# Kernel optimization log

Measured on AMD Instinct MI355X. Metric: run time of the kernel, lower is better.

Reference implementation:

```python
import jax, jax.numpy as jnp
import numpy as np

# ---- config (YOLOv4-style, TRAIN_SIZE=608, P2..P5) ----
STRIDES = (4.0, 8.0, 16.0, 32.0)
ANCHORS = np.array([
    [[12, 16], [19, 36], [40, 28], [36, 75]],
    [[36, 75], [76, 55], [72, 146], [142, 110]],
    [[72, 146], [142, 110], [192, 243], [459, 401]],
    [[142, 110], [192, 243], [300, 300], [459, 401]],
], dtype=np.float32)  # [LEVELS, NUM_ANCHORS, 2]
MAX_PROP = 100
SCORE_THRESH = 0.25
IOU_THRESH = 0.5


def decode_prediction(p, anchors, stride):
    # p: [b, A, h, w, 6] -> [b, A*h*w, 5] with xyxy + score
    b, A, h, w, _ = p.shape
    txy, twh, conf, cls = p[..., :2], p[..., 2:4], p[..., 4:5], p[..., 5:6]
    gx, gy = jnp.meshgrid(jnp.arange(w, dtype=p.dtype), jnp.arange(h, dtype=p.dtype))
    grid = jnp.stack([gx, gy], axis=-1)[None, None]  # [1,1,h,w,2]
    xy = (jax.nn.sigmoid(txy) + grid) * stride
    wh = jnp.exp(twh) * anchors[None, :, None, None, :]
    score = jax.nn.sigmoid(conf) * jax.nn.sigmoid(cls)
    x1y1 = xy - 0.5 * wh
    x2y2 = xy + 0.5 * wh
    out = jnp.concatenate([x1y1, x2y2, score], axis=-1)  # [b,A,h,w,5]
    return out.reshape(b, A * h * w, 5)


def _iou_one_vs_all(box, boxes):
    # box: [4], boxes: [N,4] (xyxy)
    lt = jnp.maximum(box[:2], boxes[:, :2])
    rb = jnp.minimum(box[2:], boxes[:, 2:])
    wh = jnp.maximum(rb - lt, 0.0)
    inter = wh[:, 0] * wh[:, 1]
    a1 = jnp.maximum(box[2] - box[0], 0.0) * jnp.maximum(box[3] - box[1], 0.0)
    a2 = jnp.maximum(boxes[:, 2] - boxes[:, 0], 0.0) * jnp.maximum(boxes[:, 3] - boxes[:, 1], 0.0)
    return inter / (a1 + a2 - inter + 1e-9)


def _nms_single(boxes, scores):
    # greedy NMS, padded to MAX_PROP with zero rows
    s0 = jnp.where(scores >= SCORE_THRESH, scores, 0.0)

    def step(s, _):
        i = jnp.argmax(s)
        sc = s[i]
        box = boxes[i]
        keep = sc > 0.0
        row = jnp.where(keep, jnp.concatenate([box, sc[None]]), jnp.zeros(5, boxes.dtype))
        iou = _iou_one_vs_all(box, boxes)
        s = jnp.where((iou > IOU_THRESH) & keep, 0.0, s)
        s = s.at[i].set(0.0)
        return s, row

    _, props = jax.lax.scan(step, s0, None, length=MAX_PROP)
    return props  # [MAX_PROP, 5]


def entry_stop_gradients(t, mask):
    # gradient flows only through entries where mask==1
    return jax.lax.stop_gradient(t) * (1.0 - mask) + t * mask


def _forward(p2, p3, p4, p5):
    anchors = jnp.asarray(ANCHORS)
    d2 = decode_prediction(p2, anchors[0], STRIDES[0])
    d3 = decode_prediction(p3, anchors[1], STRIDES[1])
    d4 = decode_prediction(p4, anchors[2], STRIDES[2])
    d5 = decode_prediction(p5, anchors[3], STRIDES[3])
    proposals = jnp.concatenate([d2, d3, d4, d5], axis=1)  # [b, N, 5]
    proposals = jax.vmap(lambda pr: _nms_single(pr[:, :4], pr[:, 4]))(proposals)  # [b, MAX_PROP, 5]
    mask = (jnp.sum(proposals[..., :4], axis=-1) != 0.0).astype(proposals.dtype)[..., None]
    return entry_stop_gradients(proposals, mask)


def setup_inputs() -> dict:
    key = jax.random.key(0)
    k2, k3, k4, k5 = jax.random.split(key, 4)
    b, A, ch = 32, 4, 6
    return {
        "p2": jax.random.normal(k2, (b, A, 152, 152, ch), dtype=jnp.float32),
        "p3": jax.random.normal(k3, (b, A, 76, 76, ch), dtype=jnp.float32),
        "p4": jax.random.normal(k4, (b, A, 38, 38, ch), dtype=jnp.float32),
        "p5": jax.random.normal(k5, (b, A, 19, 19, ch), dtype=jnp.float32),
    }


def reference(p2, p3, p4, p5):
    return _forward(p2, p3, p4, p5)
```

## Files before the change

kernel.cpp:

```cpp
#include <hip/hip_runtime.h>
#include <cstdint>
#include <cstddef>

typedef unsigned int u32;
typedef unsigned long long u64;

#define NTOT 122740
#define NQ   30685
#define NPAIR 61370
#define KTOP 1024
#define WIN  256
#define NBIN 4096
#define SCORE_T 0.25f
#define TBITS 0x3E800000u
#define CSTRIDE 64


#define WS_COUNTERS 524288
#define WS_COMPACT  532480
#define WS_SCORES   794624

__device__ __forceinline__ float sigm(float x) { return 1.0f / (1.0f + expf(-x)); }

__device__ __forceinline__ int score_bin(u32 bits) {
  return min(4095, 1 + (int)((bits - TBITS) >> 12));
}

__device__ __forceinline__ u64 shfl_u64(u64 x, int src) {
  int lo = __shfl((int)(u32)x, src, 64);
  int hi = __shfl((int)(u32)(x >> 32), src, 64);
  return ((u64)(u32)hi << 32) | (u32)lo;
}

__device__ float4 decode_box_from_gidx(u32 gidx, int b,
    const float* __restrict__ p2, const float* __restrict__ p3,
    const float* __restrict__ p4, const float* __restrict__ p5)
{
  const float* p; int t, H, W; float stride;
  float aw0, ah0, aw1, ah1, aw2, ah2, aw3, ah3;
  if (gidx < 92416u) {
    p = p2 + (size_t)b * 92416 * 6; t = (int)gidx; H = 152; W = 152; stride = 4.0f;
    aw0=12.f; ah0=16.f; aw1=19.f; ah1=36.f; aw2=40.f; ah2=28.f; aw3=36.f; ah3=75.f;
  } else if (gidx < 115520u) {
    p = p3 + (size_t)b * 23104 * 6; t = (int)(gidx - 92416u); H = 76; W = 76; stride = 8.0f;
    aw0=36.f; ah0=75.f; aw1=76.f; ah1=55.f; aw2=72.f; ah2=146.f; aw3=142.f; ah3=110.f;
  } else if (gidx < 121296u) {
    p = p4 + (size_t)b * 5776 * 6; t = (int)(gidx - 115520u); H = 38; W = 38; stride = 16.0f;
    aw0=72.f; ah0=146.f; aw1=142.f; ah1=110.f; aw2=192.f; ah2=243.f; aw3=459.f; ah3=401.f;
  } else {
    p = p5 + (size_t)b * 1444 * 6; t = (int)(gidx - 121296u); H = 19; W = 19; stride = 32.0f;
    aw0=142.f; ah0=110.f; aw1=192.f; ah1=243.f; aw2=300.f; ah2=300.f; aw3=459.f; ah3=401.f;
  }
  int HW = H * W;
  int a = t / HW;
  int r = t - a * HW;
  int y = r / W;
  int x = r - y * W;
  const float* q = p + (size_t)t * 6;
  float2 t01 = *(const float2*)(q + 0);
  float2 t23 = *(const float2*)(q + 2);
  float cx = (sigm(t01.x) + (float)x) * stride;
  float cy = (sigm(t01.y) + (float)y) * stride;
  float aw = (a == 0) ? aw0 : (a == 1) ? aw1 : (a == 2) ? aw2 : aw3;
  float ah = (a == 0) ? ah0 : (a == 1) ? ah1 : (a == 2) ? ah2 : ah3;
  float bw = expf(t23.x) * aw;
  float bh = expf(t23.y) * ah;
  return make_float4(cx - 0.5f * bw, cy - 0.5f * bh, cx + 0.5f * bw, cy + 0.5f * bh);
}

__device__ __forceinline__ bool iou_gt(float4 A, float4 B) {
  float ltx = fmaxf(A.x, B.x), lty = fmaxf(A.y, B.y);
  float rbx = fminf(A.z, B.z), rby = fminf(A.w, B.w);
  float w = fmaxf(rbx - ltx, 0.0f), h = fmaxf(rby - lty, 0.0f);
  float inter = w * h;
  float a1 = fmaxf(A.z - A.x, 0.0f) * fmaxf(A.w - A.y, 0.0f);
  float a2 = fmaxf(B.z - B.x, 0.0f) * fmaxf(B.w - B.y, 0.0f);
  float iou = inter / (a1 + a2 - inter + 1e-9f);
  return iou > 0.5f;
}

__global__ __launch_bounds__(1024)
void zero_kernel(u32* w) {
  int t = blockIdx.x * 1024 + threadIdx.x;
  if (t < 133120) w[t] = 0u;
}

__global__ __launch_bounds__(256)
void decode_score_hist(const float* __restrict__ p2, const float* __restrict__ p3,
                       const float* __restrict__ p4, const float* __restrict__ p5,
                       u32* __restrict__ scores, u32* __restrict__ hist)
{
  __shared__ u32 lhist[NBIN];
  const int tid = threadIdx.x;
  const int b = blockIdx.y;
  for (int i = tid; i < NBIN; i += 256) lhist[i] = 0u;
  __syncthreads();

  uint2* srow = (uint2*)(scores + (size_t)b * NTOT);
  const int pbase = blockIdx.x * 2048;
  #pragma unroll 2
  for (int k = 0; k < 8; ++k) {
    int P = pbase + k * 256 + tid;
    if (P < NPAIR) {
      int t0 = 2 * P;
      const float* p; int l0, LN;
      if (t0 < 92416)       { p = p2; l0 = t0;          LN = 92416; }
      else if (t0 < 115520) { p = p3; l0 = t0 - 92416;  LN = 23104; }
      else if (t0 < 121296) { p = p4; l0 = t0 - 115520; LN = 5776;  }
      else                  { p = p5; l0 = t0 - 121296; LN = 1444;  }
      const float* q = p + ((size_t)b * LN + (size_t)l0) * 6 + 4;
      float4 v1 = *(const float4*)(q);
      float4 v2 = *(const float4*)(q + 4);
      float s0 = sigm(v1.x) * sigm(v1.y);
      float s1 = sigm(v2.z) * sigm(v2.w);
      u32 b0 = (s0 >= SCORE_T) ? __float_as_uint(s0) : 0u;
      u32 b1 = (s1 >= SCORE_T) ? __float_as_uint(s1) : 0u;
      srow[P] = make_uint2(b0, b1);
      if (b0) atomicAdd(&lhist[score_bin(b0)], 1u);
      if (b1) atomicAdd(&lhist[score_bin(b1)], 1u);
    }
  }
  __syncthreads();
  u32* gh = hist + (size_t)b * NBIN;
  for (int i = tid; i < NBIN; i += 256) {
    u32 v = lhist[i];
    if (v) atomicAdd(&gh[i], v);
  }
}

__global__ __launch_bounds__(256)
void scan_kernel(u32* __restrict__ hist, u32* __restrict__ counters)
{
  __shared__ u32 shist[NBIN];
  __shared__ u32 scan[256];
  __shared__ int s_B, s_n;
  const int tid = threadIdx.x;
  const int b = blockIdx.x;
  u32* gh = hist + (size_t)b * NBIN;
  for (int i = tid; i < NBIN; i += 256) shist[i] = gh[i];
  __syncthreads();

  u32 loc[16];
  u32 g = 0;
  const int base = tid * 16;
  #pragma unroll
  for (int k = 0; k < 16; ++k) { loc[k] = shist[base + k]; g += loc[k]; }
  scan[tid] = g;
  __syncthreads();
  for (int off = 1; off < 256; off <<= 1) {
    u32 v = (tid + off < 256) ? scan[tid + off] : 0u;
    __syncthreads();
    scan[tid] += v;
    __syncthreads();
  }
  if (tid == 0 && scan[0] <= (u32)KTOP) { s_B = 1; s_n = (int)scan[0]; }
  {
    u32 nxt = (tid < 255) ? scan[tid + 1] : 0u;
    if (scan[tid] > (u32)KTOP && nxt <= (u32)KTOP) {
      u32 c = nxt; int Bv = base + 16; u32 nv = nxt;
      for (int k = 15; k >= 0; --k) {
        c += loc[k];
        if (c <= (u32)KTOP) { Bv = base + k; nv = c; } else break;
      }
      s_B = Bv; s_n = (int)nv;
    }
  }
  {
    u32 s = (tid < 255) ? scan[tid + 1] : 0u;
    for (int k = 15; k >= 0; --k) { gh[base + k] = s; s += loc[k]; }
  }
  __syncthreads();
  if (tid == 0) {
    counters[(size_t)b * CSTRIDE]     = (u32)s_n;
    counters[(size_t)b * CSTRIDE + 1] = (u32)max(s_B, 1);
  }
}

__global__ __launch_bounds__(256)
void filter_kernel(const u32* __restrict__ scores, u32* __restrict__ binpos,
                   const u32* __restrict__ counters, uint2* __restrict__ compact)
{
  const int tid = threadIdx.x;
  const int b = blockIdx.y;
  const int B = (int)counters[(size_t)b * CSTRIDE + 1];
  u32* bp = binpos + (size_t)b * NBIN;
  uint2* crow = compact + (size_t)b * KTOP;
  const uint4* sp = (const uint4*)(scores + (size_t)b * NTOT);
  const int i0 = blockIdx.x * 2048;
  const int i1 = min(i0 + 2048, NQ);
  for (int i = i0 + tid; i < i1; i += 256) {
    uint4 v = sp[i];
    u32 c4[4] = { v.x, v.y, v.z, v.w };
    #pragma unroll
    for (int c = 0; c < 4; ++c) {
      u32 bits = c4[c];
      if (bits) {
        int bin = score_bin(bits);
        if (bin >= B) {
          u32 slot = atomicAdd(&bp[bin], 1u);
          if (slot < (u32)KTOP)
            crow[slot] = make_uint2(bits, (u32)(4 * i + c));
        }
      }
    }
  }
}

__global__ __launch_bounds__(1024, 1)
void sort_nms_kernel(const uint2* __restrict__ compact, const u32* __restrict__ counters,
                     const float* __restrict__ p2, const float* __restrict__ p3,
                     const float* __restrict__ p4, const float* __restrict__ p5,
                     float* __restrict__ out)
{
  const int b = blockIdx.x;
  const int tid = threadIdx.x;

  __shared__ u64 skey[KTOP];
  __shared__ float4 sbox[WIN];
  __shared__ u64 smat[WIN * 4];
  __shared__ float4 selbox[100];
  __shared__ int s_misc[4];
  __shared__ int s_flag;

  const int n = min((int)counters[(size_t)b * CSTRIDE], KTOP);
  const uint2* crow = compact + (size_t)b * KTOP;

  if (tid < n) {
    uint2 pr = crow[tid];
    skey[tid] = ((u64)pr.x << 32) | (u32)(~pr.y);
  } else {
    skey[tid] = 0ull;
  }
  __syncthreads();

  for (int round = 0; round < 600; ++round) {
    if (tid == 0) s_flag = 0;
    __syncthreads();
    if (tid < 512) {
      int p = 2 * tid;
      u64 a = skey[p], c = skey[p + 1];
      if (a < c) { skey[p] = c; skey[p + 1] = a; s_flag = 1; }
    }
    __syncthreads();
    if (tid < 511) {
      int p = 2 * tid + 1;
      u64 a = skey[p], c = skey[p + 1];
      if (a < c) { skey[p] = c; skey[p + 1] = a; s_flag = 1; }
    }
    __syncthreads();
    int f = s_flag;
    __syncthreads();
    if (!f) break;
  }

  const int Wn = min(n, WIN);

  if (tid < WIN) {
    sbox[tid] = (tid < Wn) ? decode_box_from_gidx(~(u32)skey[tid], b, p2, p3, p4, p5)
                           : make_float4(0.f, 0.f, 0.f, 0.f);
  }
  __syncthreads();

  {
    int row = tid & 255, word = tid >> 8;
    u64 bits = 0;
    if (row < Wn) {
      float4 A = sbox[row];
      int j0 = word * 64;
      int je = min(64, Wn - j0);
      for (int j = 0; j < je; ++j)
        if (iou_gt(A, sbox[j0 + j])) bits |= (1ull << j);
    }
    smat[word * 256 + row] = bits;
  }
  __syncthreads();

  if (tid < 64) {
    const int lane = tid;
    u64 m0[4], m1[4], m2[4], m3[4];
    #pragma unroll
    for (int w = 0; w < 4; ++w) {
      m0[w] = smat[w * 256 +   0 + lane];
      m1[w] = smat[w * 256 +  64 + lane];
      m2[w] = smat[w * 256 + 128 + lane];
      m3[w] = smat[w * 256 + 192 + lane];
    }
    u64 live[4];
    #pragma unroll
    for (int g2 = 0; g2 < 4; ++g2) {
      int lo = g2 * 64;
      live[g2] = (Wn >= lo + 64) ? ~0ull : (Wn > lo ? ((1ull << (Wn - lo)) - 1ull) : 0ull);
    }
    int sel = 0;
    #pragma unroll 1
    for (int w2 = 0; w2 < 4; ++w2) {
      while (live[w2] && sel < 100) {
        int j = (int)__ffsll(live[w2]) - 1;
        int p = (w2 << 6) + j;
        u64 r0, r1, r2, r3;
        if (w2 == 0)      { r0 = shfl_u64(m0[0], j); r1 = shfl_u64(m0[1], j); r2 = shfl_u64(m0[2], j); r3 = shfl_u64(m0[3], j); }
        else if (w2 == 1) { r0 = shfl_u64(m1[0], j); r1 = shfl_u64(m1[1], j); r2 = shfl_u64(m1[2], j); r3 = shfl_u64(m1[3], j); }
        else if (w2 == 2) { r0 = shfl_u64(m2[0], j); r1 = shfl_u64(m2[1], j); r2 = shfl_u64(m2[2], j); r3 = shfl_u64(m2[3], j); }
        else              { r0 = shfl_u64(m3[0], j); r1 = shfl_u64(m3[1], j); r2 = shfl_u64(m3[2], j); r3 = shfl_u64(m3[3], j); }
        live[0] &= ~r0; live[1] &= ~r1; live[2] &= ~r2; live[3] &= ~r3;
        live[w2] &= ~(1ull << j);
        if (lane == 0) {
          float4 box = sbox[p];
          u64 k = skey[p];
          float sc = __uint_as_float((u32)(k >> 32));
          selbox[sel] = box;
          float* orow = out + (size_t)b * 500 + (size_t)sel * 5;
          orow[0] = box.x; orow[1] = box.y; orow[2] = box.z; orow[3] = box.w; orow[4] = sc;
        }
        sel++;
      }
    }
    if (lane == 0) {
      s_misc[2] = sel;
      s_misc[3] = (sel < 100 && n > WIN) ? 1 : 0;
    }
  }
  __syncthreads();

  if (s_misc[3]) {
    if (tid < 64) {
      const int lane = tid;
      int sel = s_misc[2];
      for (int p = WIN; p < n && sel < 100; ++p) {
        u64 k = skey[p];
        float4 box = decode_box_from_gidx(~(u32)k, b, p2, p3, p4, p5);
        bool hit = false;
        if (lane < sel) hit = iou_gt(selbox[lane], box);
        if (lane + 64 < sel) hit = hit || iou_gt(selbox[lane + 64], box);
        u64 anyhit = __ballot(hit);
        if (anyhit == 0ull) {
          if (lane == 0) {
            selbox[sel] = box;
            float sc = __uint_as_float((u32)(k >> 32));
            float* orow = out + (size_t)b * 500 + (size_t)sel * 5;
            orow[0] = box.x; orow[1] = box.y; orow[2] = box.z; orow[3] = box.w; orow[4] = sc;
          }
          sel++;
        }
      }
      if (lane == 0) s_misc[2] = sel;
    }
  }
  __syncthreads();

  const int nsel = s_misc[2];
  for (int i = tid; i < (100 - nsel) * 5; i += 1024)
    out[(size_t)b * 500 + (size_t)nsel * 5 + i] = 0.0f;
}

extern "C" void kernel_launch(void* const* d_in, const int* in_sizes, int n_in,
                              void* d_out, int out_size, void* d_ws, size_t ws_size,
                              hipStream_t stream) {
  const float* p2 = (const float*)d_in[0];
  const float* p3 = (const float*)d_in[1];
  const float* p4 = (const float*)d_in[2];
  const float* p5 = (const float*)d_in[3];
  float* out = (float*)d_out;

  unsigned char* w = (unsigned char*)d_ws;
  u32*   hist     = (u32*)w;
  u32*   counters = (u32*)(w + WS_COUNTERS);
  uint2* compact  = (uint2*)(w + WS_COMPACT);
  u32*   scores   = (u32*)(w + WS_SCORES);

  zero_kernel<<<130, 1024, 0, stream>>>(hist);
  decode_score_hist<<<dim3(30, 32), 256, 0, stream>>>(p2, p3, p4, p5, scores, hist);
  scan_kernel<<<32, 256, 0, stream>>>(hist, counters);
  filter_kernel<<<dim3(15, 32), 256, 0, stream>>>(scores, hist, counters, compact);
  sort_nms_kernel<<<32, 1024, 0, stream>>>(compact, counters, p2, p3, p4, p5, out);
}
```

Baseline: 189.7 us.

## Fuse scan, filter and sort-NMS into one per-batch kernel with bin-rank sort

Merges the histogram scan, top-K filter and sort/NMS stages into a single 1024-thread block per batch, keeping bin cursors and candidate keys in shared memory. The odd-even transposition sort is replaced by a rank sort within each histogram bin, which relies on bins already being ordered. The zeroing kernel becomes a memset. This removes launch overhead, global compact/counter traffic and many barrier-heavy sort rounds, but the filter pass now runs on only 32 blocks, reducing parallelism for scanning the score array.

Measured after the change: 184.6 us. 1.03x faster.

```diff
diff --git a/kernel.cpp b/kernel.cpp
--- a/kernel.cpp
+++ b/kernel.cpp
@@ -13,12 +13,9 @@
 #define NBIN 4096
 #define SCORE_T 0.25f
 #define TBITS 0x3E800000u
-#define CSTRIDE 64
-
-
-#define WS_COUNTERS 524288
-#define WS_COMPACT  532480
-#define WS_SCORES   794624
+
+
+#define WS_SCORES 524288
 
 __device__ __forceinline__ float sigm(float x) { return 1.0f / (1.0f + expf(-x)); }
 
@@ -77,12 +74,6 @@
   float a2 = fmaxf(B.z - B.x, 0.0f) * fmaxf(B.w - B.y, 0.0f);
   float iou = inter / (a1 + a2 - inter + 1e-9f);
   return iou > 0.5f;
-}
-
-__global__ __launch_bounds__(1024)
-void zero_kernel(u32* w) {
-  int t = blockIdx.x * 1024 + threadIdx.x;
-  if (t < 133120) w[t] = 0u;
 }
 
 __global__ __launch_bounds__(256)
@@ -128,35 +119,50 @@
   }
 }
 
-__global__ __launch_bounds__(256)
-void scan_kernel(u32* __restrict__ hist, u32* __restrict__ counters)
+__global__ __launch_bounds__(1024, 1)
+void mega_kernel(const u32* __restrict__ scores, const u32* __restrict__ hist,
+                 const float* __restrict__ p2, const float* __restrict__ p3,
+                 const float* __restrict__ p4, const float* __restrict__ p5,
+                 float* __restrict__ out)
 {
-  __shared__ u32 shist[NBIN];
-  __shared__ u32 scan[256];
+  const int b = blockIdx.x;
+  const int tid = threadIdx.x;
+
+  __shared__ u32 sstart[NBIN];
+  __shared__ u32 scur[NBIN];
+  __shared__ u32 sscan[256];
+  __shared__ u64 skey[KTOP];
+  __shared__ u64 skey2[KTOP];
+  __shared__ float4 sbox[WIN];
+  __shared__ u64 smat[WIN * 4];
+  __shared__ float4 selbox[100];
+  __shared__ int s_misc[4];
   __shared__ int s_B, s_n;
-  const int tid = threadIdx.x;
-  const int b = blockIdx.x;
-  u32* gh = hist + (size_t)b * NBIN;
-  for (int i = tid; i < NBIN; i += 256) shist[i] = gh[i];
-  __syncthreads();
-
-  u32 loc[16];
-  u32 g = 0;
-  const int base = tid * 16;
-  #pragma unroll
-  for (int k = 0; k < 16; ++k) { loc[k] = shist[base + k]; g += loc[k]; }
-  scan[tid] = g;
+
+  const u32* gh = hist + (size_t)b * NBIN;
+  for (int i = tid; i < NBIN; i += 1024) scur[i] = gh[i];
+  __syncthreads();
+
+  u32 loc[16]; int base = 0;
+  if (tid < 256) {
+    base = tid * 16;
+    u32 g = 0;
+    #pragma unroll
+    for (int k = 0; k < 16; ++k) { loc[k] = scur[base + k]; g += loc[k]; }
+    sscan[tid] = g;
+  }
   __syncthreads();
   for (int off = 1; off < 256; off <<= 1) {
-    u32 v = (tid + off < 256) ? scan[tid + off] : 0u;
+    u32 v = 0;
+    if (tid < 256) v = (tid + off < 256) ? sscan[tid + off] : 0u;
     __syncthreads();
-    scan[tid] += v;
+    if (tid < 256) sscan[tid] += v;
     __syncthreads();
   }
-  if (tid == 0 && scan[0] <= (u32)KTOP) { s_B = 1; s_n = (int)scan[0]; }
-  {
-    u32 nxt = (tid < 255) ? scan[tid + 1] : 0u;
-    if (scan[tid] > (u32)KTOP && nxt <= (u32)KTOP) {
+  if (tid == 0 && sscan[0] <= (u32)KTOP) { s_B = 1; s_n = (int)sscan[0]; }
+  if (tid < 256) {
+    u32 nxt = (tid < 255) ? sscan[tid + 1] : 0u;
+    if (sscan[tid] > (u32)KTOP && nxt <= (u32)KTOP) {
       u32 c = nxt; int Bv = base + 16; u32 nv = nxt;
       for (int k = 15; k >= 0; --k) {
         c += loc[k];
@@ -164,99 +170,69 @@
       }
       s_B = Bv; s_n = (int)nv;
     }
-  }
+    u32 s = nxt;
+    for (int k = 15; k >= 0; --k) { sstart[base + k] = s; s += loc[k]; }
+  }
+  __syncthreads();
+  const int B = max(s_B, 1);
+  const int n = min(s_n, KTOP);
+
+  for (int i = tid; i < NBIN; i += 1024) scur[i] = sstart[i];
+  skey[tid] = 0ull;
+  skey2[tid] = 0ull;
+  __syncthreads();
+
   {
-    u32 s = (tid < 255) ? scan[tid + 1] : 0u;
-    for (int k = 15; k >= 0; --k) { gh[base + k] = s; s += loc[k]; }
-  }
-  __syncthreads();
-  if (tid == 0) {
-    counters[(size_t)b * CSTRIDE]     = (u32)s_n;
-    counters[(size_t)b * CSTRIDE + 1] = (u32)max(s_B, 1);
-  }
-}
-
-__global__ __launch_bounds__(256)
-void filter_kernel(const u32* __restrict__ scores, u32* __restrict__ binpos,
-                   const u32* __restrict__ counters, uint2* __restrict__ compact)
-{
-  const int tid = threadIdx.x;
-  const int b = blockIdx.y;
-  const int B = (int)counters[(size_t)b * CSTRIDE + 1];
-  u32* bp = binpos + (size_t)b * NBIN;
-  uint2* crow = compact + (size_t)b * KTOP;
-  const uint4* sp = (const uint4*)(scores + (size_t)b * NTOT);
-  const int i0 = blockIdx.x * 2048;
-  const int i1 = min(i0 + 2048, NQ);
-  for (int i = i0 + tid; i < i1; i += 256) {
-    uint4 v = sp[i];
-    u32 c4[4] = { v.x, v.y, v.z, v.w };
-    #pragma unroll
-    for (int c = 0; c < 4; ++c) {
-      u32 bits = c4[c];
-      if (bits) {
-        int bin = score_bin(bits);
-        if (bin >= B) {
-          u32 slot = atomicAdd(&bp[bin], 1u);
-          if (slot < (u32)KTOP)
-            crow[slot] = make_uint2(bits, (u32)(4 * i + c));
+    const uint4* sp = (const uint4*)(scores + (size_t)b * NTOT);
+    #pragma unroll 1
+    for (int kk = 0; kk < 8; ++kk) {
+      int i0 = kk * 4096 + tid;
+      uint4 v0, v1, v2, v3;
+      bool g0 = (i0        < NQ), g1 = (i0 + 1024 < NQ);
+      bool g2 = (i0 + 2048 < NQ), g3 = (i0 + 3072 < NQ);
+      if (g0) v0 = sp[i0];
+      if (g1) v1 = sp[i0 + 1024];
+      if (g2) v2 = sp[i0 + 2048];
+      if (g3) v3 = sp[i0 + 3072];
+      #pragma unroll
+      for (int q = 0; q < 4; ++q) {
+        bool gq = (q == 0) ? g0 : (q == 1) ? g1 : (q == 2) ? g2 : g3;
+        if (!gq) continue;
+        uint4 v = (q == 0) ? v0 : (q == 1) ? v1 : (q == 2) ? v2 : v3;
+        int ii = i0 + q * 1024;
+        u32 c4[4] = { v.x, v.y, v.z, v.w };
+        #pragma unroll
+        for (int c = 0; c < 4; ++c) {
+          u32 bits = c4[c];
+          if (bits) {
+            int bin = score_bin(bits);
+            if (bin >= B) {
+              u32 slot = atomicAdd(&scur[bin], 1u);
+              if (slot < (u32)KTOP)
+                skey[slot] = ((u64)bits << 32) | (u32)(~(u32)(4 * ii + c));
+            }
+          }
         }
       }
     }
   }
-}
-
-__global__ __launch_bounds__(1024, 1)
-void sort_nms_kernel(const uint2* __restrict__ compact, const u32* __restrict__ counters,
-                     const float* __restrict__ p2, const float* __restrict__ p3,
-                     const float* __restrict__ p4, const float* __restrict__ p5,
-                     float* __restrict__ out)
-{
-  const int b = blockIdx.x;
-  const int tid = threadIdx.x;
-
-  __shared__ u64 skey[KTOP];
-  __shared__ float4 sbox[WIN];
-  __shared__ u64 smat[WIN * 4];
-  __shared__ float4 selbox[100];
-  __shared__ int s_misc[4];
-  __shared__ int s_flag;
-
-  const int n = min((int)counters[(size_t)b * CSTRIDE], KTOP);
-  const uint2* crow = compact + (size_t)b * KTOP;
-
-  if (tid < n) {
-    uint2 pr = crow[tid];
-    skey[tid] = ((u64)pr.x << 32) | (u32)(~pr.y);
-  } else {
-    skey[tid] = 0ull;
-  }
-  __syncthreads();
-
-  for (int round = 0; round < 600; ++round) {
-    if (tid == 0) s_flag = 0;
-    __syncthreads();
-    if (tid < 512) {
-      int p = 2 * tid;
-      u64 a = skey[p], c = skey[p + 1];
-      if (a < c) { skey[p] = c; skey[p + 1] = a; s_flag = 1; }
-    }
-    __syncthreads();
-    if (tid < 511) {
-      int p = 2 * tid + 1;
-      u64 a = skey[p], c = skey[p + 1];
-      if (a < c) { skey[p] = c; skey[p + 1] = a; s_flag = 1; }
-    }
-    __syncthreads();
-    int f = s_flag;
-    __syncthreads();
-    if (!f) break;
-  }
+  __syncthreads();
+
+  for (int s = tid; s < n; s += 1024) {
+    u64 k = skey[s];
+    int bin = score_bin((u32)(k >> 32));
+    int st = (int)sstart[bin];
+    int en = (int)scur[bin];
+    u32 r = 0;
+    for (int j = st; j < en; ++j) r += (skey[j] > k) ? 1u : 0u;
+    skey2[st + r] = k;
+  }
+  __syncthreads();
 
   const int Wn = min(n, WIN);
 
   if (tid < WIN) {
-    sbox[tid] = (tid < Wn) ? decode_box_from_gidx(~(u32)skey[tid], b, p2, p3, p4, p5)
+    sbox[tid] = (tid < Wn) ? decode_box_from_gidx(~(u32)skey2[tid], b, p2, p3, p4, p5)
                            : make_float4(0.f, 0.f, 0.f, 0.f);
   }
   __syncthreads();
@@ -306,7 +282,7 @@
         live[w2] &= ~(1ull << j);
         if (lane == 0) {
           float4 box = sbox[p];
-          u64 k = skey[p];
+          u64 k = skey2[p];
           float sc = __uint_as_float((u32)(k >> 32));
           selbox[sel] = box;
           float* orow = out + (size_t)b * 500 + (size_t)sel * 5;
@@ -327,7 +303,7 @@
       const int lane = tid;
       int sel = s_misc[2];
       for (int p = WIN; p < n && sel < 100; ++p) {
-        u64 k = skey[p];
+        u64 k = skey2[p];
         float4 box = decode_box_from_gidx(~(u32)k, b, p2, p3, p4, p5);
         bool hit = false;
         if (lane < sel) hit = iou_gt(selbox[lane], box);
@@ -363,14 +339,10 @@
   float* out = (float*)d_out;
 
   unsigned char* w = (unsigned char*)d_ws;
-  u32*   hist     = (u32*)w;
-  u32*   counters = (u32*)(w + WS_COUNTERS);
-  uint2* compact  = (uint2*)(w + WS_COMPACT);
-  u32*   scores   = (u32*)(w + WS_SCORES);
-
-  zero_kernel<<<130, 1024, 0, stream>>>(hist);
+  u32* hist   = (u32*)w;
+  u32* scores = (u32*)(w + WS_SCORES);
+
+  hipMemsetAsync(hist, 0, 32 * NBIN * sizeof(u32), stream);
   decode_score_hist<<<dim3(30, 32), 256, 0, stream>>>(p2, p3, p4, p5, scores, hist);
-  scan_kernel<<<32, 256, 0, stream>>>(hist, counters);
-  filter_kernel<<<dim3(15, 32), 256, 0, stream>>>(scores, hist, counters, compact);
-  sort_nms_kernel<<<32, 1024, 0, stream>>>(compact, counters, p2, p3, p4, p5, out);
-}
+  mega_kernel<<<32, 1024, 0, stream>>>(scores, hist, p2, p3, p4, p5, out);
+}
```
